# Optimization experiments

Hardware: AMD Instinct MI355X
Metric: run time of the kernel (lower is better)

## Reference

```python
import jax, jax.numpy as jnp
import numpy as np

THRESHOLD = 0.9  # graph_threshold; graph_secondary is None
EPS = 1e-12


def setup_inputs() -> dict:
    key = jax.random.key(0)
    k_x, k_cw, k_cb, k_u, k_lw, k_lb = jax.random.split(key, 6)
    B = 8192
    x = jax.random.normal(k_x, (B, 1, 28, 28), dtype=jnp.float32)
    conv_w = jax.random.normal(k_cw, (4, 1, 2, 2), dtype=jnp.float32) * 0.5  # OIHW
    conv_b = jax.random.normal(k_cb, (4,), dtype=jnp.float32) * 0.1
    # random orthogonal 4x4 "quantum" unitary via QR, as in the torch buffer
    unitary = jnp.linalg.qr(jax.random.normal(k_u, (4, 4), dtype=jnp.float32))[0]
    D = 4 * 14 * 14  # conv_out * num_patches = 784
    lin_w = jax.random.normal(k_lw, (10, D), dtype=jnp.float32) * (1.0 / np.sqrt(D))
    lin_b = jax.random.normal(k_lb, (10,), dtype=jnp.float32) * 0.01
    return {"x": x, "conv_w": conv_w, "conv_b": conv_b, "unitary": unitary,
            "lin_w": lin_w, "lin_b": lin_b}


def _forward(x, conv_w, conv_b, unitary, lin_w, lin_b):
    B = x.shape[0]
    # _PatchConv: 2x2 conv, stride 2, then flatten to [B, 4*14*14]
    feats = jax.lax.conv_general_dilated(
        x, conv_w, window_strides=(2, 2), padding="VALID",
        dimension_numbers=("NCHW", "OIHW", "NCHW"))
    feats = feats + conv_b[None, :, None, None]
    flat = feats.reshape(B, -1)                      # [B, 784]
    # _QuantumPatchEncoder: reinterpret as [B, 196, 4], apply unitary^T
    patches = flat.reshape(B, -1, 4)
    qf = jnp.einsum("bnk,wk->bnw", patches, unitary).reshape(B, -1)  # [B, 784]
    # linear head + log_softmax
    logits = qf @ lin_w.T + lin_b
    log_probs = jax.nn.log_softmax(logits, axis=-1)
    # GraphAdjacencyLayer: pairwise squared-cosine fidelity, thresholded.
    # Vectorized: normalize rows, one GEMM, square, threshold.
    qn = qf / (jnp.linalg.norm(qf, axis=-1, keepdims=True) + EPS)   # [B, 784]
    fid = (qn @ qn.T) ** 2                                          # [B, B]
    adj = jnp.where(fid >= THRESHOLD, 1.0, 0.0).astype(jnp.float32)
    adj = adj * (1.0 - jnp.eye(B, dtype=jnp.float32))  # no self-edges (i<j pairs)
    return log_probs, adj


def reference(x, conv_w, conv_b, unitary, lin_w, lin_b):
    return _forward(x, conv_w, conv_b, unitary, lin_w, lin_b)
```

## Files before the change

kernel.cpp:

```cpp
#include <hip/hip_runtime.h>
#include <hip/hip_bf16.h>

typedef unsigned char uchar_t;
typedef __attribute__((ext_vector_type(4)))  float f32x4;
typedef __attribute__((ext_vector_type(16))) float f32x16;

#define B_SZ 8192
#define D_FT 784
#define N_KT 13
#define PLANE_U32 131072
#define PLANE_B   524288
#define THRESH 0.9f

#define GLOBAL_AS(p) ((const __attribute__((address_space(1))) void*)(p))
#define LDS_AS(p)    ((__attribute__((address_space(3))) void*)(p))

__global__ __launch_bounds__(256) void preproc_kernel(
    const float* __restrict__ x, const float* __restrict__ conv_w,
    const float* __restrict__ conv_b, const float* __restrict__ unitary,
    const float* __restrict__ lin_w, const float* __restrict__ lin_b,
    float* __restrict__ log_probs, uchar_t* __restrict__ qn)
{
    __shared__ float xr[4][784];
    __shared__ float qf[4][784];

    const int t = threadIdx.x, lane = t & 63, wave = t >> 6;
    const int b = blockIdx.x * 4 + wave;
    float* xw = xr[wave];
    float* qw = qf[wave];

    const float4* xsrc = (const float4*)(x + (size_t)b * 784);
    #pragma unroll
    for (int i = lane; i < 196; i += 64) ((float4*)xw)[i] = xsrc[i];
    __syncthreads();

    float sumsq = 0.f;
    for (int g = lane; g < 196; g += 64) {
        const int c = g / 49, p = g % 49;
        const float w00 = conv_w[c*4+0], w01 = conv_w[c*4+1];
        const float w10 = conv_w[c*4+2], w11 = conv_w[c*4+3];
        const float bcv = conv_b[c];
        float feat[4];
        #pragma unroll
        for (int j = 0; j < 4; ++j) {
            const int s = 4*p + j;
            const int h = s / 14, wq = s % 14;
            const float* px = &xw[(2*h)*28 + 2*wq];
            feat[j] = bcv + w00*px[0] + w01*px[1] + w10*px[28] + w11*px[29];
        }
        #pragma unroll
        for (int w = 0; w < 4; ++w) {
            float v = unitary[w*4+0]*feat[0] + unitary[w*4+1]*feat[1]
                    + unitary[w*4+2]*feat[2] + unitary[w*4+3]*feat[3];
            qw[4*g + w] = v;
            sumsq += v * v;
        }
    }
    __syncthreads();

    #pragma unroll
    for (int off = 1; off < 64; off <<= 1) sumsq += __shfl_xor(sumsq, off, 64);
    const float inv = 1.0f / (sqrtf(sumsq) + 1e-12f);

    unsigned int* qbase = (unsigned int*)qn;
    for (int i = lane; i < 208; i += 64) {
        unsigned int o = 0u;
        if (i < 196) {
            const float v0 = qw[4*i+0] * inv, v1 = qw[4*i+1] * inv;
            const float v2 = qw[4*i+2] * inv, v3 = qw[4*i+3] * inv;
            int lo = __builtin_amdgcn_cvt_pk_fp8_f32(v0, v1, 0, 0);
            o = (unsigned int)__builtin_amdgcn_cvt_pk_fp8_f32(v2, v3, lo, 1);
        }
        qbase[(size_t)(i >> 4) * PLANE_U32 + (size_t)b * 16 + (i & 15)] = o;
    }

    float acc[10];
    #pragma unroll
    for (int cl = 0; cl < 10; ++cl) acc[cl] = 0.f;
    for (int k = lane; k < 784; k += 64) {
        const float v = qw[k];
        #pragma unroll
        for (int cl = 0; cl < 10; ++cl) acc[cl] += v * lin_w[cl*784 + k];
    }
    #pragma unroll
    for (int cl = 0; cl < 10; ++cl) {
        #pragma unroll
        for (int off = 1; off < 64; off <<= 1)
            acc[cl] += __shfl_xor(acc[cl], off, 64);
        acc[cl] += lin_b[cl];
    }
    if (lane == 0) {
        float mx = -1e30f;
        #pragma unroll
        for (int cl = 0; cl < 10; ++cl) mx = fmaxf(mx, acc[cl]);
        float se = 0.f;
        #pragma unroll
        for (int cl = 0; cl < 10; ++cl) se += expf(acc[cl] - mx);
        const float lse = mx + logf(se);
        #pragma unroll
        for (int cl = 0; cl < 10; ++cl)
            log_probs[(size_t)b*10 + cl] = acc[cl] - lse;
    }
}

__global__ __launch_bounds__(512, 2) void gram_kernel(
    const uchar_t* __restrict__ qn, float* __restrict__ adj)
{
    const int t0 = blockIdx.x;
    int tl = (t0 & 7) * 66 + (t0 >> 3);
    int br = (int)((65.0 - sqrt(4225.0 - 8.0 * (double)tl)) * 0.5);
    while ((br + 1) * (65 - (br + 1)) / 2 <= tl) ++br;
    while (br * (65 - br) / 2 > tl) --br;
    const int bc = br + (tl - br * (65 - br) / 2);

    __shared__ uchar_t ldsA[3][16384] __attribute__((aligned(16)));
    __shared__ uchar_t ldsB[3][16384] __attribute__((aligned(16)));

    const int t = threadIdx.x;
    const int lane = t & 63, wave = t >> 6;
    const int wrow = wave >> 1, wcol = wave & 1;
    const int l32 = lane & 31, half = lane >> 5;

    const bool offdiag = (br != bc);
    const int br256 = br * 256, bc256 = bc * 256;
    const int zmask = offdiag ? 32767 : 16383;

    const int srow = lane & 15, sck = (lane >> 4) * 16;
    const uchar_t* gA0 = qn + (size_t)(br256 + wave*16       + srow) * 64 + sck;
    const uchar_t* gA1 = qn + (size_t)(br256 + (wave+8)*16   + srow) * 64 + sck;
    const uchar_t* gB0 = qn + (size_t)(bc256 + wave*16       + srow) * 64 + sck;
    const uchar_t* gB1 = qn + (size_t)(bc256 + (wave+8)*16   + srow) * 64 + sck;
    const int ld0 = wave * 1024, ld1 = (wave + 8) * 1024;

    #define STAGE(p, koff) do {                                                            \
        __builtin_amdgcn_global_load_lds(GLOBAL_AS(gA0 + (koff)), LDS_AS(&ldsA[p][ld0]), 16, 0, 0); \
        __builtin_amdgcn_global_load_lds(GLOBAL_AS(gA1 + (koff)), LDS_AS(&ldsA[p][ld1]), 16, 0, 0); \
        __builtin_amdgcn_global_load_lds(GLOBAL_AS(gB0 + (koff)), LDS_AS(&ldsB[p][ld0]), 16, 0, 0); \
        __builtin_amdgcn_global_load_lds(GLOBAL_AS(gB1 + (koff)), LDS_AS(&ldsB[p][ld1]), 16, 0, 0); \
    } while (0)

    int aoff[2], boff[4];
    #pragma unroll
    for (int mi = 0; mi < 2; ++mi) {
        const int r = wrow*64 + mi*32 + l32;
        aoff[mi] = (r >> 4)*1024 + (r & 15)*16 + half*8;
    }
    #pragma unroll
    for (int ni = 0; ni < 4; ++ni) {
        const int c = wcol*128 + ni*32 + l32;
        boff[ni] = (c >> 4)*1024 + (c & 15)*16 + half*8;
    }

    f32x16 acc[2][4] = {};
    STAGE(0, 0);
    STAGE(1, PLANE_B);

    #pragma unroll
    for (int kt = 0; kt < N_KT; ++kt) {
        const int p = kt % 3, p2 = (kt + 2) % 3;

        asm volatile("" ::: "memory");
        if (kt == 0)               __builtin_amdgcn_s_waitcnt(0xF74);
        else if (kt == 1)          __builtin_amdgcn_s_waitcnt(0xF79);
        else if (kt == N_KT - 1)   __builtin_amdgcn_s_waitcnt(0xF7A);
        else                       __builtin_amdgcn_s_waitcnt(0xF7E);
        __builtin_amdgcn_s_barrier();
        asm volatile("" ::: "memory");

        if (kt + 2 < N_KT) STAGE(p2, (size_t)(kt + 2) * PLANE_B);
        asm volatile("" ::: "memory");

        {
            f32x4 z = {0.f, 0.f, 0.f, 0.f};
            #pragma unroll
            for (int j = 0; j < 5; ++j) {
                const int idx  = (kt * 2560 + j * 512 + t) & zmask;
                const int tile = idx >> 14;
                const int r    = (idx >> 6) & 255;
                const int c4   = idx & 63;
                const int rowb = tile ? bc256 : br256;
                const int colb = tile ? br256 : bc256;
                __builtin_nontemporal_store(
                    z, (f32x4*)adj + (size_t)(rowb + r) * 2048 + (colb >> 2) + c4);
            }
        }
        asm volatile("" ::: "memory");

        #pragma unroll
        for (int s = 0; s < 4; ++s) {
            long a0 = *(const long*)&ldsA[p][aoff[0] + s*256];
            long a1 = *(const long*)&ldsA[p][aoff[1] + s*256];
            long b0 = *(const long*)&ldsB[p][boff[0] + s*256];
            long b1 = *(const long*)&ldsB[p][boff[1] + s*256];
            long b2 = *(const long*)&ldsB[p][boff[2] + s*256];
            long b3 = *(const long*)&ldsB[p][boff[3] + s*256];
            acc[0][0] = __builtin_amdgcn_mfma_f32_32x32x16_fp8_fp8(a0, b0, acc[0][0], 0, 0, 0);
            acc[1][0] = __builtin_amdgcn_mfma_f32_32x32x16_fp8_fp8(a1, b0, acc[1][0], 0, 0, 0);
            acc[0][1] = __builtin_amdgcn_mfma_f32_32x32x16_fp8_fp8(a0, b1, acc[0][1], 0, 0, 0);
            acc[1][1] = __builtin_amdgcn_mfma_f32_32x32x16_fp8_fp8(a1, b1, acc[1][1], 0, 0, 0);
            acc[0][2] = __builtin_amdgcn_mfma_f32_32x32x16_fp8_fp8(a0, b2, acc[0][2], 0, 0, 0);
            acc[1][2] = __builtin_amdgcn_mfma_f32_32x32x16_fp8_fp8(a1, b2, acc[1][2], 0, 0, 0);
            acc[0][3] = __builtin_amdgcn_mfma_f32_32x32x16_fp8_fp8(a0, b3, acc[0][3], 0, 0, 0);
            acc[1][3] = __builtin_amdgcn_mfma_f32_32x32x16_fp8_fp8(a1, b3, acc[1][3], 0, 0, 0);
        }
    }
    #undef STAGE

    asm volatile("" ::: "memory");
    __builtin_amdgcn_s_waitcnt(0xF70);
    __builtin_amdgcn_s_barrier();
    asm volatile("" ::: "memory");

    #pragma unroll
    for (int mi = 0; mi < 2; ++mi) {
        const int rbase = br256 + wrow*64 + mi*32 + 4*half;
        #pragma unroll
        for (int ni = 0; ni < 4; ++ni) {
            const int gc = bc256 + wcol*128 + ni*32 + l32;
            const f32x16 v = acc[mi][ni];
            #pragma unroll
            for (int q = 0; q < 4; ++q) {
                const int gr0 = rbase + 8*q;
                float o[4];
                bool h = false;
                #pragma unroll
                for (int r = 0; r < 4; ++r) {
                    const float val = v[4*q + r];
                    o[r] = (val*val >= THRESH && (gr0 + r) != gc) ? 1.0f : 0.0f;
                    h = h || (o[r] != 0.0f);
                }
                if (__any(h)) {
                    #pragma unroll
                    for (int r = 0; r < 4; ++r)
                        adj[(size_t)(gr0 + r) * B_SZ + gc] = o[r];
                    if (offdiag)
                        *(float4*)&adj[(size_t)gc * B_SZ + gr0] =
                            make_float4(o[0], o[1], o[2], o[3]);
                }
            }
        }
    }
}

extern "C" void kernel_launch(void* const* d_in, const int* in_sizes, int n_in,
                              void* d_out, int out_size, void* d_ws, size_t ws_size,
                              hipStream_t stream) {
    const float* x       = (const float*)d_in[0];
    const float* conv_w  = (const float*)d_in[1];
    const float* conv_b  = (const float*)d_in[2];
    const float* unitary = (const float*)d_in[3];
    const float* lin_w   = (const float*)d_in[4];
    const float* lin_b   = (const float*)d_in[5];

    float* log_probs = (float*)d_out;
    float* adj       = (float*)d_out + (size_t)B_SZ * 10;
    uchar_t* qn      = (uchar_t*)d_ws;

    preproc_kernel<<<B_SZ / 4, 256, 0, stream>>>(x, conv_w, conv_b, unitary,
                                                 lin_w, lin_b, log_probs, qn);
    gram_kernel<<<528, 512, 0, stream>>>(qn, adj);
}
```

Before: 346.4 us.

## Double-buffer two K-planes per barrier phase instead of triple-buffering single planes

Restructures the gram kernel main loop from 13 single-plane steps with a 3-deep LDS ring into 7 phases that each hold two K-planes in a 2-deep double buffer. This halves the number of barriers and waitcnt points and doubles the MFMA work between syncs. The zero-fill stores per phase double to match, and they switch from nontemporal to normal stores. The cost is a shallower prefetch distance and a larger LDS footprint (128KB), which could limit occupancy to fewer blocks per CU.

```diff
diff --git a/kernel.cpp b/kernel.cpp
--- a/kernel.cpp
+++ b/kernel.cpp
@@ -7,7 +7,7 @@
 
 #define B_SZ 8192
 #define D_FT 784
-#define N_KT 13
+#define N_PH 7
 #define PLANE_U32 131072
 #define PLANE_B   524288
 #define THRESH 0.9f
@@ -113,8 +113,8 @@
     while (br * (65 - br) / 2 > tl) --br;
     const int bc = br + (tl - br * (65 - br) / 2);
 
-    __shared__ uchar_t ldsA[3][16384] __attribute__((aligned(16)));
-    __shared__ uchar_t ldsB[3][16384] __attribute__((aligned(16)));
+    __shared__ uchar_t ldsA[2][32768] __attribute__((aligned(16)));
+    __shared__ uchar_t ldsB[2][32768] __attribute__((aligned(16)));
 
     const int t = threadIdx.x;
     const int lane = t & 63, wave = t >> 6;
@@ -132,11 +132,13 @@
     const uchar_t* gB1 = qn + (size_t)(bc256 + (wave+8)*16   + srow) * 64 + sck;
     const int ld0 = wave * 1024, ld1 = (wave + 8) * 1024;
 
-    #define STAGE(p, koff) do {                                                            \
-        __builtin_amdgcn_global_load_lds(GLOBAL_AS(gA0 + (koff)), LDS_AS(&ldsA[p][ld0]), 16, 0, 0); \
-        __builtin_amdgcn_global_load_lds(GLOBAL_AS(gA1 + (koff)), LDS_AS(&ldsA[p][ld1]), 16, 0, 0); \
-        __builtin_amdgcn_global_load_lds(GLOBAL_AS(gB0 + (koff)), LDS_AS(&ldsB[p][ld0]), 16, 0, 0); \
-        __builtin_amdgcn_global_load_lds(GLOBAL_AS(gB1 + (koff)), LDS_AS(&ldsB[p][ld1]), 16, 0, 0); \
+    #define STAGE1(p, reg, plane) do {                                                     \
+        const size_t ko = (size_t)(plane) * PLANE_B;                                       \
+        const int ro = (reg) * 16384;                                                      \
+        __builtin_amdgcn_global_load_lds(GLOBAL_AS(gA0 + ko), LDS_AS(&ldsA[p][ro + ld0]), 16, 0, 0); \
+        __builtin_amdgcn_global_load_lds(GLOBAL_AS(gA1 + ko), LDS_AS(&ldsA[p][ro + ld1]), 16, 0, 0); \
+        __builtin_amdgcn_global_load_lds(GLOBAL_AS(gB0 + ko), LDS_AS(&ldsB[p][ro + ld0]), 16, 0, 0); \
+        __builtin_amdgcn_global_load_lds(GLOBAL_AS(gB1 + ko), LDS_AS(&ldsB[p][ro + ld1]), 16, 0, 0); \
     } while (0)
 
     int aoff[2], boff[4];
@@ -152,48 +154,49 @@
     }
 
     f32x16 acc[2][4] = {};
-    STAGE(0, 0);
-    STAGE(1, PLANE_B);
-
-    #pragma unroll
-    for (int kt = 0; kt < N_KT; ++kt) {
-        const int p = kt % 3, p2 = (kt + 2) % 3;
-
-        asm volatile("" ::: "memory");
-        if (kt == 0)               __builtin_amdgcn_s_waitcnt(0xF74);
-        else if (kt == 1)          __builtin_amdgcn_s_waitcnt(0xF79);
-        else if (kt == N_KT - 1)   __builtin_amdgcn_s_waitcnt(0xF7A);
-        else                       __builtin_amdgcn_s_waitcnt(0xF7E);
+    STAGE1(0, 0, 0);
+    STAGE1(0, 1, 1);
+
+    #pragma unroll
+    for (int ph = 0; ph < N_PH; ++ph) {
+        const int p = ph & 1;
+
+        asm volatile("" ::: "memory");
+        if (ph == 0) __builtin_amdgcn_s_waitcnt(0xF70);
+        else         __builtin_amdgcn_s_waitcnt(0xF7A);
         __builtin_amdgcn_s_barrier();
         asm volatile("" ::: "memory");
 
-        if (kt + 2 < N_KT) STAGE(p2, (size_t)(kt + 2) * PLANE_B);
+        if (ph < 5) { STAGE1(p ^ 1, 0, 2*ph + 2); STAGE1(p ^ 1, 1, 2*ph + 3); }
+        else if (ph == 5) { STAGE1(p ^ 1, 0, 12); }
         asm volatile("" ::: "memory");
 
         {
             f32x4 z = {0.f, 0.f, 0.f, 0.f};
             #pragma unroll
-            for (int j = 0; j < 5; ++j) {
-                const int idx  = (kt * 2560 + j * 512 + t) & zmask;
+            for (int j = 0; j < 10; ++j) {
+                const int idx  = (ph * 5120 + j * 512 + t) & zmask;
                 const int tile = idx >> 14;
                 const int r    = (idx >> 6) & 255;
                 const int c4   = idx & 63;
                 const int rowb = tile ? bc256 : br256;
                 const int colb = tile ? br256 : bc256;
-                __builtin_nontemporal_store(
-                    z, (f32x4*)adj + (size_t)(rowb + r) * 2048 + (colb >> 2) + c4);
+                *((f32x4*)adj + (size_t)(rowb + r) * 2048 + (colb >> 2) + c4) = z;
             }
         }
         asm volatile("" ::: "memory");
 
-        #pragma unroll
-        for (int s = 0; s < 4; ++s) {
-            long a0 = *(const long*)&ldsA[p][aoff[0] + s*256];
-            long a1 = *(const long*)&ldsA[p][aoff[1] + s*256];
-            long b0 = *(const long*)&ldsB[p][boff[0] + s*256];
-            long b1 = *(const long*)&ldsB[p][boff[1] + s*256];
-            long b2 = *(const long*)&ldsB[p][boff[2] + s*256];
-            long b3 = *(const long*)&ldsB[p][boff[3] + s*256];
+        const int nks = (ph == 6) ? 4 : 8;
+        #pragma unroll
+        for (int ks = 0; ks < 8; ++ks) {
+            if (ks >= nks) break;
+            const int ro = (ks >> 2) * 16384, s = ks & 3;
+            long a0 = *(const long*)&ldsA[p][ro + aoff[0] + s*256];
+            long a1 = *(const long*)&ldsA[p][ro + aoff[1] + s*256];
+            long b0 = *(const long*)&ldsB[p][ro + boff[0] + s*256];
+            long b1 = *(const long*)&ldsB[p][ro + boff[1] + s*256];
+            long b2 = *(const long*)&ldsB[p][ro + boff[2] + s*256];
+            long b3 = *(const long*)&ldsB[p][ro + boff[3] + s*256];
             acc[0][0] = __builtin_amdgcn_mfma_f32_32x32x16_fp8_fp8(a0, b0, acc[0][0], 0, 0, 0);
             acc[1][0] = __builtin_amdgcn_mfma_f32_32x32x16_fp8_fp8(a1, b0, acc[1][0], 0, 0, 0);
             acc[0][1] = __builtin_amdgcn_mfma_f32_32x32x16_fp8_fp8(a0, b1, acc[0][1], 0, 0, 0);
@@ -204,7 +207,7 @@
             acc[1][3] = __builtin_amdgcn_mfma_f32_32x32x16_fp8_fp8(a1, b3, acc[1][3], 0, 0, 0);
         }
     }
-    #undef STAGE
+    #undef STAGE1
 
     asm volatile("" ::: "memory");
     __builtin_amdgcn_s_waitcnt(0xF70);
```

New measurement: 367.2 us. +6.0%, slower.
